# Performance work log

Measured on AMD Instinct MI355X. Metric: run time of the kernel, lower is better.

The kernel has to match this reference:

```python
import jax, jax.numpy as jnp
import numpy as np

B, NQ, NK = 16, 512, 1024
CQ, CV = 128, 128
H, D = 8, 64            # nb_heads, attention_size
SCALE = float(np.sqrt(D))


def setup_inputs() -> dict:
    key = jax.random.key(0)
    ks = jax.random.split(key, 10)
    s = 0.02
    return {
        "query": jax.random.normal(ks[0], (B, NQ, CQ), jnp.float32),
        "key": jax.random.normal(ks[1], (B, NK, CV), jnp.float32),
        "c_mask": jax.random.randint(ks[2], (B, NK), 0, 2).astype(jnp.float32),
        # torch Linear params, stored as [in, out] so y = x @ W + b
        "Wq": jax.random.normal(ks[3], (CQ, H * D), jnp.float32) * s,
        "bq": jnp.zeros((H * D,), jnp.float32),
        "Wk": jax.random.normal(ks[4], (CV, H * D), jnp.float32) * s,
        "bk": jnp.zeros((H * D,), jnp.float32),
        "Wv": jax.random.normal(ks[5], (CV, H * D), jnp.float32) * s,
        "bv": jnp.zeros((H * D,), jnp.float32),
    }


def reference(query, key, c_mask, Wq, bq, Wk, bk, Wv, bv):
    # projections -> [B, N, H, D]
    q = (query @ Wq + bq).reshape(B, NQ, H, D)
    k = (key @ Wk + bk).reshape(B, NK, H, D)
    v = (key @ Wv + bv).reshape(B, NK, H, D)
    # scaled scores [B, H, NQ, NK]
    scores = jnp.einsum('bqhd,bkhd->bhqk', q / SCALE, k)
    # additive mask: c_mask [B, NK] broadcasts over heads and queries
    scores = scores - 100000.0 * (1.0 - c_mask[:, None, None, :])
    attn = jax.nn.softmax(scores, axis=-1)
    # weighted values -> [B, NQ, H, D] -> concat heads
    c = jnp.einsum('bhqk,bkhd->bqhd', attn, v)
    return c.reshape(B, NQ, H * D)
```

## Files before the change

kernel.cpp:

```cpp
#include <hip/hip_runtime.h>
#include <hip/hip_bf16.h>

#define B_  16
#define NQ_ 512
#define NK_ 1024
#define CQ_ 128
#define H_  8
#define D_  64
#define HD_ 512

typedef __attribute__((ext_vector_type(8))) short short8;
typedef __attribute__((ext_vector_type(4))) float floatx4;

__device__ __forceinline__ short f2bf(float f) {
    union { float f; unsigned u; } x; x.f = f;
    unsigned r = (x.u + 0x7fffu + ((x.u >> 16) & 1u)) >> 16;
    return (short)r;
}
__device__ __forceinline__ int f2bf_pk(float a, float b) {
    __hip_bfloat162 h = __float22bfloat162_rn(make_float2(a, b));
    int r; __builtin_memcpy(&r, &h, 4); return r;
}
__device__ __forceinline__ void async16(const short* g, short* l) {
    __builtin_amdgcn_global_load_lds(
        (const __attribute__((address_space(1))) void*)g,
        (__attribute__((address_space(3))) void*)l, 16, 0, 0);
}

__global__ void prep_kernel(const float* __restrict__ W0, const float* __restrict__ W1,
                            const float* __restrict__ W2, short* __restrict__ T0,
                            short* __restrict__ T1, short* __restrict__ T2,
                            const float* __restrict__ query, const float* __restrict__ key_,
                            short* __restrict__ xq, short* __restrict__ xk) {
    int gi = blockIdx.x * blockDim.x + threadIdx.x;
    if (gi < 196608) {
        int sel = gi >> 16;
        int idx = gi & 65535;
        const float* W = sel == 0 ? W0 : (sel == 1 ? W1 : W2);
        short* T = sel == 0 ? T0 : (sel == 1 ? T1 : T2);
        int n = idx >> 7, k = idx & 127;
        T[idx] = f2bf(W[k * HD_ + n]);
        return;
    }
    int gi2 = gi - 196608;
    const float* src; short* dst; int idx;
    if (gi2 < 262144) { src = query; dst = xq; idx = gi2; }
    else              { src = key_;  dst = xk; idx = gi2 - 262144; }
    float4 v = *(const float4*)(src + (size_t)idx * 4);
    *(int2*)(dst + (size_t)idx * 4) = make_int2(f2bf_pk(v.x, v.y), f2bf_pk(v.z, v.w));
}

__global__ __launch_bounds__(256) void proj7_kernel(
    const short* __restrict__ xq, const short* __restrict__ xk,
    const short* __restrict__ wqt, const short* __restrict__ wkt,
    const short* __restrict__ wvt,
    const float* __restrict__ bq, const float* __restrict__ bk,
    const float* __restrict__ bv,
    short* __restrict__ qs, short* __restrict__ ks, short* __restrict__ vt,
    float qscale)
{
    __shared__ __align__(16) short csh[9216];

    int bx = blockIdx.x;
    const short* X; const short* Wt; const float* bias; short* out;
    int rshift, transposed; float scale;
    if (bx < 64)       { X = xq; Wt = wqt; bias = bq; out = qs; rshift = 9;  scale = qscale; transposed = 0; }
    else if (bx < 192) { bx -= 64;  X = xk; Wt = wkt; bias = bk; out = ks; rshift = 10; scale = 1.0f; transposed = 0; }
    else               { bx -= 192; X = xk; Wt = wvt; bias = bv; out = vt; rshift = 10; scale = 1.0f; transposed = 1; }

    const int tid  = threadIdx.x;
    const int w    = tid >> 6, lane = tid & 63;
    const int l15  = lane & 15, quad = lane >> 4;
    const int mbase = bx * 128;

    short8 afr[2][4];
    #pragma unroll
    for (int mt = 0; mt < 2; ++mt) {
        const short* xrow = X + (size_t)(mbase + w * 32 + mt * 16 + l15) * CQ_;
        #pragma unroll
        for (int kt = 0; kt < 4; ++kt)
            afr[mt][kt] = *(const short8*)(xrow + kt * 32 + quad * 8);
    }

    const int rows = 1 << rshift;
    const int b  = mbase >> rshift;
    const int r0 = mbase & (rows - 1);

    #pragma unroll
    for (int hh = 0; hh < 2; ++hh) {
        const int h = blockIdx.y * 2 + hh;
        short8 bfr[4][4];
        #pragma unroll
        for (int nt = 0; nt < 4; ++nt) {
            const short8* wrow = (const short8*)(Wt + (size_t)(h * 64 + nt * 16 + l15) * CQ_);
            #pragma unroll
            for (int kt = 0; kt < 4; ++kt) bfr[nt][kt] = wrow[kt * 4 + quad];
        }
        floatx4 acc[2][4];
        #pragma unroll
        for (int mt = 0; mt < 2; ++mt)
            #pragma unroll
            for (int nt = 0; nt < 4; ++nt) {
                floatx4 a = {0.f, 0.f, 0.f, 0.f};
                #pragma unroll
                for (int kt = 0; kt < 4; ++kt)
                    a = __builtin_amdgcn_mfma_f32_16x16x32_bf16(afr[mt][kt], bfr[nt][kt], a, 0, 0, 0);
                acc[mt][nt] = a;
            }
        __syncthreads();
        #pragma unroll
        for (int mt = 0; mt < 2; ++mt)
            #pragma unroll
            for (int nt = 0; nt < 4; ++nt) {
                const float bvv = bias[h * 64 + nt * 16 + l15];
                #pragma unroll
                for (int i = 0; i < 4; ++i) {
                    const short s = f2bf((acc[mt][nt][i] + bvv) * scale);
                    const int m = w * 32 + mt * 16 + quad * 4 + i;
                    const int n = nt * 16 + l15;
                    if (!transposed) csh[m * 72 + n]  = s;
                    else             csh[n * 136 + m] = s;
                }
            }
        __syncthreads();

        const size_t bh = (size_t)(b * H_ + h);
        if (!transposed) {
            short* dst = out + (bh * rows + r0) * D_;
            #pragma unroll
            for (int it = 0; it < 4; ++it) {
                const int idx = it * 256 + tid;
                const int row = idx >> 3, c8 = (idx & 7) * 8;
                *(short8*)(dst + idx * 8) = *(const short8*)&csh[row * 72 + c8];
            }
        } else {
            short* dst = out + bh * D_ * NK_ + r0;
            #pragma unroll
            for (int it = 0; it < 4; ++it) {
                const int idx = it * 256 + tid;
                const int row = idx >> 4, c8 = (idx & 15) * 8;
                *(short8*)(dst + (size_t)row * NK_ + c8) = *(const short8*)&csh[row * 136 + c8];
            }
        }
    }
}

__global__ __launch_bounds__(256) void attn_kernel(
    const short* __restrict__ qs, const short* __restrict__ ks,
    const short* __restrict__ vt, const float* __restrict__ cmask,
    float* __restrict__ out)
{
    __shared__ __align__(16) short kbuf[2][64 * 64];
    __shared__ __align__(16) short vbuf[2][64 * 64];
    __shared__ __align__(16) short psh[128 * 64];

    const int tid = threadIdx.x;
    const int w = tid >> 6, lane = tid & 63;
    const int l15 = lane & 15, quad = lane >> 4;

    const int bx   = blockIdx.x;
    const int xcd  = bx & 7;
    const int r_   = bx >> 3;
    const int qblk = r_ & 3;
    const int bh_i = (r_ >> 2) * 8 + xcd;
    const int h    = bh_i & 7;
    const int b    = bh_i >> 3;

    const size_t bh = (size_t)bh_i;
    const short* qb  = qs + (bh * NQ_ + (size_t)qblk * 128 + w * 32) * D_;
    const short* kb_ = ks + bh * NK_ * D_;
    const short* vb  = vt + bh * D_ * NK_;
    const float* mk  = cmask + (size_t)b * NK_;

    short8 qa[2][2];
    #pragma unroll
    for (int g = 0; g < 2; ++g) {
        const short8* qrow = (const short8*)(qb + (size_t)(g * 16 + l15) * D_);
        qa[g][0] = qrow[quad];
        qa[g][1] = qrow[4 + quad];
    }

    const int srow8 = lane >> 3, sc = lane & 7;

    float l_lane[2] = {0.f, 0.f};
    floatx4 o_acc[2][4];
    #pragma unroll
    for (int g = 0; g < 2; ++g)
        #pragma unroll
        for (int dt = 0; dt < 4; ++dt) o_acc[g][dt] = (floatx4){0.f, 0.f, 0.f, 0.f};

    #pragma unroll
    for (int j = 0; j < 2; ++j) {
        const int row = w * 16 + j * 8 + srow8;
        const int cs = sc ^ (row & 7);
        async16(kb_ + (size_t)row * D_ + cs * 8, &kbuf[0][(w * 16 + j * 8) * 64]);
        async16(vb + (size_t)row * NK_ + cs * 8, &vbuf[0][(w * 16 + j * 8) * 64]);
    }
    __syncthreads();

    for (int t = 0; t < 16; ++t) {
        const int cur = t & 1;
        if (t < 15) {
            const int nb = (t + 1) * 64, nxt = cur ^ 1;
            #pragma unroll
            for (int j = 0; j < 2; ++j) {
                const int row = w * 16 + j * 8 + srow8;
                const int cs = sc ^ (row & 7);
                async16(kb_ + (size_t)(nb + row) * D_ + cs * 8, &kbuf[nxt][(w * 16 + j * 8) * 64]);
                async16(vb + (size_t)row * NK_ + nb + cs * 8, &vbuf[nxt][(w * 16 + j * 8) * 64]);
            }
        }
        const short* kb = kbuf[cur];
        const short* vbl = vbuf[cur];
        const int kbase = t * 64;

        short8 ka[4][2];
        #pragma unroll
        for (int nt = 0; nt < 4; ++nt) {
            const int row = nt * 16 + l15;
            ka[nt][0] = *(const short8*)&kb[row * 64 + ((quad    ) ^ (row & 7)) * 8];
            ka[nt][1] = *(const short8*)&kb[row * 64 + ((4 + quad) ^ (row & 7)) * 8];
        }
        short8 vf[2][4];
        #pragma unroll
        for (int dt = 0; dt < 4; ++dt) {
            const int row = dt * 16 + l15;
            vf[0][dt] = *(const short8*)&vbl[row * 64 + ((quad    ) ^ (row & 7)) * 8];
            vf[1][dt] = *(const short8*)&vbl[row * 64 + ((4 + quad) ^ (row & 7)) * 8];
        }
        float4 m4[4];
        #pragma unroll
        for (int nt = 0; nt < 4; ++nt)
            m4[nt] = *(const float4*)(mk + kbase + nt * 16 + quad * 4);

        #pragma unroll
        for (int g = 0; g < 2; ++g) {
            floatx4 st[4];
            #pragma unroll
            for (int nt = 0; nt < 4; ++nt) {
                floatx4 a = {0.f, 0.f, 0.f, 0.f};
                a = __builtin_amdgcn_mfma_f32_16x16x32_bf16(ka[nt][1], qa[g][1], a, 0, 0, 0);
                a = __builtin_amdgcn_mfma_f32_16x16x32_bf16(ka[nt][0], qa[g][0], a, 0, 0, 0);
                st[nt] = a;
            }
            const int prow = w * 32 + g * 16 + l15;
            float psum = 0.f;
            #pragma unroll
            for (int nt = 0; nt < 4; ++nt) {
                float p0 = m4[nt].x * __builtin_amdgcn_exp2f(st[nt][0]);
                float p1 = m4[nt].y * __builtin_amdgcn_exp2f(st[nt][1]);
                float p2 = m4[nt].z * __builtin_amdgcn_exp2f(st[nt][2]);
                float p3 = m4[nt].w * __builtin_amdgcn_exp2f(st[nt][3]);
                psum += (p0 + p1) + (p2 + p3);
                int2 pk = make_int2(f2bf_pk(p0, p1), f2bf_pk(p2, p3));
                const int c16 = (2 * nt + (quad >> 1)) ^ (prow & 7);
                *(int2*)&psh[prow * 64 + c16 * 8 + (quad & 1) * 4] = pk;
            }
            l_lane[g] += psum;
        }
        #pragma unroll
        for (int g = 0; g < 2; ++g) {
            const int prow = w * 32 + g * 16 + l15;
            #pragma unroll
            for (int kt = 0; kt < 2; ++kt) {
                short8 pa = *(const short8*)&psh[prow * 64 + ((kt * 4 + quad) ^ (prow & 7)) * 8];
                #pragma unroll
                for (int dt = 0; dt < 4; ++dt)
                    o_acc[g][dt] = __builtin_amdgcn_mfma_f32_16x16x32_bf16(vf[kt][dt], pa, o_acc[g][dt], 0, 0, 0);
            }
        }
        __syncthreads();
    }

    #pragma unroll
    for (int g = 0; g < 2; ++g) {
        float ls = l_lane[g];
        ls += __shfl_xor(ls, 16);
        ls += __shfl_xor(ls, 32);
        const float linv = 1.0f / ls;
        const int qr = qblk * 128 + w * 32 + g * 16 + l15;
        float* orow = out + ((size_t)b * NQ_ + qr) * HD_ + h * D_;
        #pragma unroll
        for (int dt = 0; dt < 4; ++dt) {
            float4 v = make_float4(o_acc[g][dt][0] * linv, o_acc[g][dt][1] * linv,
                                   o_acc[g][dt][2] * linv, o_acc[g][dt][3] * linv);
            *(float4*)(orow + dt * 16 + quad * 4) = v;
        }
    }
}

extern "C" void kernel_launch(void* const* d_in, const int* in_sizes, int n_in,
                              void* d_out, int out_size, void* d_ws, size_t ws_size,
                              hipStream_t stream) {
    const float* query = (const float*)d_in[0];
    const float* key   = (const float*)d_in[1];
    const float* cmask = (const float*)d_in[2];
    const float* Wq    = (const float*)d_in[3];
    const float* bq    = (const float*)d_in[4];
    const float* Wk    = (const float*)d_in[5];
    const float* bk    = (const float*)d_in[6];
    const float* Wv    = (const float*)d_in[7];
    const float* bv    = (const float*)d_in[8];
    float* out = (float*)d_out;

    char* ws = (char*)d_ws;
    short* qs  = (short*)(ws);
    short* ks  = (short*)(ws + (size_t)( 8u << 20));
    short* vt  = (short*)(ws + (size_t)(24u << 20));
    char*  w40 = ws + (size_t)(40u << 20);
    short* wqt = (short*)(w40);
    short* wkt = (short*)(w40 + 131072 * 2);
    short* wvt = (short*)(w40 + 131072 * 4);
    short* xq  = (short*)(w40 + 131072 * 6);
    short* xk  = (short*)(w40 + 131072 * 6 + (2u << 20));

    prep_kernel<<<dim3(3840), dim3(256), 0, stream>>>(
        Wq, Wk, Wv, wqt, wkt, wvt, query, key, xq, xk);

    const float qscale = 0.125f * 1.44269504f;
    proj7_kernel<<<dim3(320, 4), dim3(256), 0, stream>>>(
        xq, xk, wqt, wkt, wvt, bq, bk, bv, qs, ks, vt, qscale);

    attn_kernel<<<dim3(512), dim3(256), 0, stream>>>(qs, ks, vt, cmask, out);
}
```

Measured before the change: 156.9 us.

## Fuse Q projection into attention and drop separate input bf16 conversion pass

Q projection now runs inside the attention kernel: each block converts its fp32 query rows to bf16 in registers, multiplies by the pre-scaled transposed Wq with MFMA, and stages the result through shared memory, so the qs intermediate is never written to or read from global memory. The K/V projection reads fp32 key directly and packs to bf16 in registers, removing the xq/xk conversion pass. The Q scale is folded into Wq and bq in the prep kernel. The block-to-head mapping changes (the XCD-aware swizzle is removed), launch bounds request 2 blocks per CU, and the two per-group loops in the PV stage are merged. In exchange, Q is recomputed per attention block and Wq is reloaded per block.

```diff
diff --git a/kernel.cpp b/kernel.cpp
--- a/kernel.cpp
+++ b/kernel.cpp
@@ -21,6 +21,15 @@
     __hip_bfloat162 h = __float22bfloat162_rn(make_float2(a, b));
     int r; __builtin_memcpy(&r, &h, 4); return r;
 }
+__device__ __forceinline__ short8 pack8(float4 a, float4 b) {
+    union { int4 i; short8 s; } u;
+    u.i = make_int4(f2bf_pk(a.x, a.y), f2bf_pk(a.z, a.w),
+                    f2bf_pk(b.x, b.y), f2bf_pk(b.z, b.w));
+    return u.s;
+}
+__device__ __forceinline__ int2 packi2(floatx4 a) {
+    return make_int2(f2bf_pk(a[0], a[1]), f2bf_pk(a[2], a[3]));
+}
 __device__ __forceinline__ void async16(const short* g, short* l) {
     __builtin_amdgcn_global_load_lds(
         (const __attribute__((address_space(1))) void*)g,
@@ -30,43 +39,35 @@
 __global__ void prep_kernel(const float* __restrict__ W0, const float* __restrict__ W1,
                             const float* __restrict__ W2, short* __restrict__ T0,
                             short* __restrict__ T1, short* __restrict__ T2,
-                            const float* __restrict__ query, const float* __restrict__ key_,
-                            short* __restrict__ xq, short* __restrict__ xk) {
+                            const float* __restrict__ bq, float* __restrict__ bqs,
+                            float qscale) {
     int gi = blockIdx.x * blockDim.x + threadIdx.x;
     if (gi < 196608) {
         int sel = gi >> 16;
         int idx = gi & 65535;
         const float* W = sel == 0 ? W0 : (sel == 1 ? W1 : W2);
         short* T = sel == 0 ? T0 : (sel == 1 ? T1 : T2);
+        float s = sel == 0 ? qscale : 1.0f;
         int n = idx >> 7, k = idx & 127;
-        T[idx] = f2bf(W[k * HD_ + n]);
+        T[idx] = f2bf(W[k * HD_ + n] * s);
         return;
     }
-    int gi2 = gi - 196608;
-    const float* src; short* dst; int idx;
-    if (gi2 < 262144) { src = query; dst = xq; idx = gi2; }
-    else              { src = key_;  dst = xk; idx = gi2 - 262144; }
-    float4 v = *(const float4*)(src + (size_t)idx * 4);
-    *(int2*)(dst + (size_t)idx * 4) = make_int2(f2bf_pk(v.x, v.y), f2bf_pk(v.z, v.w));
-}
-
-__global__ __launch_bounds__(256) void proj7_kernel(
-    const short* __restrict__ xq, const short* __restrict__ xk,
-    const short* __restrict__ wqt, const short* __restrict__ wkt,
-    const short* __restrict__ wvt,
-    const float* __restrict__ bq, const float* __restrict__ bk,
-    const float* __restrict__ bv,
-    short* __restrict__ qs, short* __restrict__ ks, short* __restrict__ vt,
-    float qscale)
+    int j = gi - 196608;
+    if (j < HD_) bqs[j] = bq[j] * qscale;
+}
+
+__global__ __launch_bounds__(256, 2) void kvproj_kernel(
+    const float* __restrict__ key_,
+    const short* __restrict__ wkt, const short* __restrict__ wvt,
+    const float* __restrict__ bk, const float* __restrict__ bv,
+    short* __restrict__ ks, short* __restrict__ vt)
 {
     __shared__ __align__(16) short csh[9216];
 
     int bx = blockIdx.x;
-    const short* X; const short* Wt; const float* bias; short* out;
-    int rshift, transposed; float scale;
-    if (bx < 64)       { X = xq; Wt = wqt; bias = bq; out = qs; rshift = 9;  scale = qscale; transposed = 0; }
-    else if (bx < 192) { bx -= 64;  X = xk; Wt = wkt; bias = bk; out = ks; rshift = 10; scale = 1.0f; transposed = 0; }
-    else               { bx -= 192; X = xk; Wt = wvt; bias = bv; out = vt; rshift = 10; scale = 1.0f; transposed = 1; }
+    const short* Wt; const float* bias; short* out; int transposed;
+    if (bx < 128) { Wt = wkt; bias = bk; out = ks; transposed = 0; }
+    else { bx -= 128; Wt = wvt; bias = bv; out = vt; transposed = 1; }
 
     const int tid  = threadIdx.x;
     const int w    = tid >> 6, lane = tid & 63;
@@ -76,15 +77,15 @@
     short8 afr[2][4];
     #pragma unroll
     for (int mt = 0; mt < 2; ++mt) {
-        const short* xrow = X + (size_t)(mbase + w * 32 + mt * 16 + l15) * CQ_;
+        const float* xrow = key_ + (size_t)(mbase + w * 32 + mt * 16 + l15) * CQ_;
         #pragma unroll
         for (int kt = 0; kt < 4; ++kt)
-            afr[mt][kt] = *(const short8*)(xrow + kt * 32 + quad * 8);
-    }
-
-    const int rows = 1 << rshift;
-    const int b  = mbase >> rshift;
-    const int r0 = mbase & (rows - 1);
+            afr[mt][kt] = pack8(*(const float4*)(xrow + kt * 32 + quad * 8),
+                                *(const float4*)(xrow + kt * 32 + quad * 8 + 4));
+    }
+
+    const int b  = mbase >> 10;
+    const int r0 = mbase & 1023;
 
     #pragma unroll
     for (int hh = 0; hh < 2; ++hh) {
@@ -115,7 +116,7 @@
                 const float bvv = bias[h * 64 + nt * 16 + l15];
                 #pragma unroll
                 for (int i = 0; i < 4; ++i) {
-                    const short s = f2bf((acc[mt][nt][i] + bvv) * scale);
+                    const short s = f2bf(acc[mt][nt][i] + bvv);
                     const int m = w * 32 + mt * 16 + quad * 4 + i;
                     const int n = nt * 16 + l15;
                     if (!transposed) csh[m * 72 + n]  = s;
@@ -126,7 +127,7 @@
 
         const size_t bh = (size_t)(b * H_ + h);
         if (!transposed) {
-            short* dst = out + (bh * rows + r0) * D_;
+            short* dst = out + (bh * NK_ + r0) * D_;
             #pragma unroll
             for (int it = 0; it < 4; ++it) {
                 const int idx = it * 256 + tid;
@@ -145,9 +146,10 @@
     }
 }
 
-__global__ __launch_bounds__(256) void attn_kernel(
-    const short* __restrict__ qs, const short* __restrict__ ks,
+__global__ __launch_bounds__(256, 2) void attn_kernel(
+    const float* __restrict__ query, const short* __restrict__ ks,
     const short* __restrict__ vt, const float* __restrict__ cmask,
+    const short* __restrict__ wqt, const float* __restrict__ bqs,
     float* __restrict__ out)
 {
     __shared__ __align__(16) short kbuf[2][64 * 64];
@@ -159,25 +161,47 @@
     const int l15 = lane & 15, quad = lane >> 4;
 
     const int bx   = blockIdx.x;
-    const int xcd  = bx & 7;
-    const int r_   = bx >> 3;
-    const int qblk = r_ & 3;
-    const int bh_i = (r_ >> 2) * 8 + xcd;
+    const int bh_i = bx & 127;
+    const int qq   = bx >> 7;
     const int h    = bh_i & 7;
     const int b    = bh_i >> 3;
 
     const size_t bh = (size_t)bh_i;
-    const short* qb  = qs + (bh * NQ_ + (size_t)qblk * 128 + w * 32) * D_;
     const short* kb_ = ks + bh * NK_ * D_;
     const short* vb  = vt + bh * D_ * NK_;
     const float* mk  = cmask + (size_t)b * NK_;
 
     short8 qa[2][2];
-    #pragma unroll
-    for (int g = 0; g < 2; ++g) {
-        const short8* qrow = (const short8*)(qb + (size_t)(g * 16 + l15) * D_);
-        qa[g][0] = qrow[quad];
-        qa[g][1] = qrow[4 + quad];
+    {
+        short8 waf[4][4];
+        #pragma unroll
+        for (int dt = 0; dt < 4; ++dt)
+            #pragma unroll
+            for (int kt = 0; kt < 4; ++kt)
+                waf[dt][kt] = *(const short8*)(wqt + (size_t)(h * 64 + dt * 16 + l15) * CQ_ + kt * 32 + quad * 8);
+        const int qr0 = qq * 128 + w * 32;
+        #pragma unroll
+        for (int g = 0; g < 2; ++g) {
+            const float* qrow = query + ((size_t)b * NQ_ + qr0 + g * 16 + l15) * CQ_;
+            short8 bqf[4];
+            #pragma unroll
+            for (int kt = 0; kt < 4; ++kt)
+                bqf[kt] = pack8(*(const float4*)(qrow + kt * 32 + quad * 8),
+                                *(const float4*)(qrow + kt * 32 + quad * 8 + 4));
+            const int prow = w * 32 + g * 16 + l15;
+            #pragma unroll
+            for (int dt = 0; dt < 4; ++dt) {
+                float4 bi = *(const float4*)(bqs + h * 64 + dt * 16 + quad * 4);
+                floatx4 a = {bi.x, bi.y, bi.z, bi.w};
+                #pragma unroll
+                for (int kt = 0; kt < 4; ++kt)
+                    a = __builtin_amdgcn_mfma_f32_16x16x32_bf16(waf[dt][kt], bqf[kt], a, 0, 0, 0);
+                const int c16 = (dt * 2 + (quad >> 1)) ^ (prow & 7);
+                *(int2*)&psh[prow * 64 + c16 * 8 + (quad & 1) * 4] = packi2(a);
+            }
+            qa[g][0] = *(const short8*)&psh[prow * 64 + ((quad    ) ^ (prow & 7)) * 8];
+            qa[g][1] = *(const short8*)&psh[prow * 64 + ((4 + quad) ^ (prow & 7)) * 8];
+        }
     }
 
     const int srow8 = lane >> 3, sc = lane & 7;
@@ -257,10 +281,6 @@
                 *(int2*)&psh[prow * 64 + c16 * 8 + (quad & 1) * 4] = pk;
             }
             l_lane[g] += psum;
-        }
-        #pragma unroll
-        for (int g = 0; g < 2; ++g) {
-            const int prow = w * 32 + g * 16 + l15;
             #pragma unroll
             for (int kt = 0; kt < 2; ++kt) {
                 short8 pa = *(const short8*)&psh[prow * 64 + ((kt * 4 + quad) ^ (prow & 7)) * 8];
@@ -278,7 +298,7 @@
         ls += __shfl_xor(ls, 16);
         ls += __shfl_xor(ls, 32);
         const float linv = 1.0f / ls;
-        const int qr = qblk * 128 + w * 32 + g * 16 + l15;
+        const int qr = qq * 128 + w * 32 + g * 16 + l15;
         float* orow = out + ((size_t)b * NQ_ + qr) * HD_ + h * D_;
         #pragma unroll
         for (int dt = 0; dt < 4; ++dt) {
@@ -304,22 +324,21 @@
     float* out = (float*)d_out;
 
     char* ws = (char*)d_ws;
-    short* qs  = (short*)(ws);
-    short* ks  = (short*)(ws + (size_t)( 8u << 20));
-    short* vt  = (short*)(ws + (size_t)(24u << 20));
-    char*  w40 = ws + (size_t)(40u << 20);
-    short* wqt = (short*)(w40);
-    short* wkt = (short*)(w40 + 131072 * 2);
-    short* wvt = (short*)(w40 + 131072 * 4);
-    short* xq  = (short*)(w40 + 131072 * 6);
-    short* xk  = (short*)(w40 + 131072 * 6 + (2u << 20));
-
-    prep_kernel<<<dim3(3840), dim3(256), 0, stream>>>(
-        Wq, Wk, Wv, wqt, wkt, wvt, query, key, xq, xk);
+    short* ks  = (short*)(ws);
+    short* vt  = (short*)(ws + (size_t)(16u << 20));
+    char*  w32 = ws + (size_t)(32u << 20);
+    short* wqt = (short*)(w32);
+    short* wkt = (short*)(w32 + 131072);
+    short* wvt = (short*)(w32 + 131072 * 2);
+    float* bqs = (float*)(w32 + 131072 * 3);
 
     const float qscale = 0.125f * 1.44269504f;
-    proj7_kernel<<<dim3(320, 4), dim3(256), 0, stream>>>(
-        xq, xk, wqt, wkt, wvt, bq, bk, bv, qs, ks, vt, qscale);
-
-    attn_kernel<<<dim3(512), dim3(256), 0, stream>>>(qs, ks, vt, cmask, out);
-}
+    prep_kernel<<<dim3(771), dim3(256), 0, stream>>>(
+        Wq, Wk, Wv, wqt, wkt, wvt, bq, bqs, qscale);
+
+    kvproj_kernel<<<dim3(256, 4), dim3(256), 0, stream>>>(
+        key, wkt, wvt, bk, bv, ks, vt);
+
+    attn_kernel<<<dim3(512), dim3(256), 0, stream>>>(
+        query, ks, vt, cmask, wqt, bqs, out);
+}
```

Result: faster. 147.6 us (-5.9%).
